# Kernel optimization log

Measured on AMD Instinct MI355X. Metric: run time of the kernel, lower is better.

Reference implementation:

```python
import jax, jax.numpy as jnp
import numpy as np

EPS = 1e-8

def setup_inputs() -> dict:
    key = jax.random.key(0)
    k1, k2 = jax.random.split(key)
    B, D, H, W, K = 32, 256, 64, 64, 64
    X = jax.random.normal(k1, (B, D, H, W), dtype=jnp.float32)
    std1 = 1.0 / float(np.sqrt(K * D))
    codewords = jax.random.uniform(k2, (K, D), dtype=jnp.float32, minval=-std1, maxval=std1)
    return {"X": X, "codewords": codewords}

def reference(X, codewords):
    B, D = X.shape[0], X.shape[1]
    # (B, D, H, W) -> (B, N, D)
    Xf = X.reshape(B, D, -1).transpose(0, 2, 1)
    # pairwise cosine similarity: normalize then matmul -> (B, N, K)
    Xn = Xf / jnp.maximum(jnp.linalg.norm(Xf, axis=-1, keepdims=True), EPS)
    Cn = codewords / jnp.maximum(jnp.linalg.norm(codewords, axis=-1, keepdims=True), EPS)
    L = jnp.einsum('bnd,kd->bnk', Xn, Cn)
    A = jax.nn.softmax(L, axis=2)
    # aggregate: E[b,k,d] = sum_n A[b,n,k] * (Xf[b,n,d] - C[k,d])
    # expressed without materializing the (B,N,K,D) residual tensor:
    E = jnp.einsum('bnk,bnd->bkd', A, Xf) - A.sum(axis=1)[:, :, None] * codewords[None, :, :]
    return E
```

## Files before the change

kernel.cpp:

```cpp
#include <hip/hip_runtime.h>
#include <hip/hip_bf16.h>
#include <math.h>

#define BB 32
#define DD 256
#define NN 4096
#define KK 64
#define EPSV 1e-8f
#define XSTR 264

typedef __attribute__((ext_vector_type(8))) short short8;
typedef __attribute__((ext_vector_type(4))) float f32x4;

__device__ __forceinline__ unsigned int bf16pair(float a, float b) {
    __hip_bfloat162 h = __float22bfloat162_rn(make_float2(a, b));
    return *(unsigned int*)&h;
}
__device__ __forceinline__ unsigned short bf16one(float a) {
    unsigned int ua = __float_as_uint(a);
    ua += 0x7fffu + ((ua >> 16) & 1u);
    return (unsigned short)(ua >> 16);
}

__device__ __forceinline__ void stage_group(int dbase, int n4, const float4* rr,
                                            unsigned short* xnd_s, unsigned short* xdn_s,
                                            f32x4& ssn) {
    float4 r0 = rr[0], r1 = rr[1], r2 = rr[2], r3 = rr[3];
    ssn.x = fmaf(r0.x, r0.x, ssn.x); ssn.x = fmaf(r1.x, r1.x, ssn.x);
    ssn.x = fmaf(r2.x, r2.x, ssn.x); ssn.x = fmaf(r3.x, r3.x, ssn.x);
    ssn.y = fmaf(r0.y, r0.y, ssn.y); ssn.y = fmaf(r1.y, r1.y, ssn.y);
    ssn.y = fmaf(r2.y, r2.y, ssn.y); ssn.y = fmaf(r3.y, r3.y, ssn.y);
    ssn.z = fmaf(r0.z, r0.z, ssn.z); ssn.z = fmaf(r1.z, r1.z, ssn.z);
    ssn.z = fmaf(r2.z, r2.z, ssn.z); ssn.z = fmaf(r3.z, r3.z, ssn.z);
    ssn.w = fmaf(r0.w, r0.w, ssn.w); ssn.w = fmaf(r1.w, r1.w, ssn.w);
    ssn.w = fmaf(r2.w, r2.w, ssn.w); ssn.w = fmaf(r3.w, r3.w, ssn.w);
#pragma unroll
    for (int j = 0; j < 4; j++) {
        int d = dbase + j;
        uint2 u;
        u.x = bf16pair(rr[j].x, rr[j].y);
        u.y = bf16pair(rr[j].z, rr[j].w);
        *(uint2*)(xdn_s + d * 64 + ((((n4 >> 3) ^ (d & 7)) << 3) | (n4 & 7))) = u;
    }
    {
        float col[4][4] = {{r0.x, r1.x, r2.x, r3.x},
                           {r0.y, r1.y, r2.y, r3.y},
                           {r0.z, r1.z, r2.z, r3.z},
                           {r0.w, r1.w, r2.w, r3.w}};
#pragma unroll
        for (int j = 0; j < 4; j++) {
            int n = n4 + j;
            uint2 u;
            u.x = bf16pair(col[j][0], col[j][1]);
            u.y = bf16pair(col[j][2], col[j][3]);
            int blk = (dbase >> 3) ^ ((n >> 2) & 3);
            *(uint2*)(xnd_s + n * XSTR + (blk << 3) + (dbase & 7)) = u;
        }
    }
}

__global__ __launch_bounds__(256, 2) void k_fused(const float* __restrict__ X,
                                                  const float* __restrict__ C,
                                                  float* __restrict__ P,
                                                  float* __restrict__ Sp) {
    __shared__ unsigned short xnd_s[64 * XSTR];
    __shared__ unsigned short xdn_s[DD * 64];
    __shared__ unsigned short at_s[KK * 72];
    __shared__ float rn4[4 * 64];
    __shared__ float red_s[4 * 64];

    int t = threadIdx.x;
    int b = blockIdx.x >> 4, chunk = blockIdx.x & 15;
    int w = t >> 6, lane = t & 63, c = lane & 15, g = lane >> 4;
    int q = t >> 4;
    int n4 = c * 4;

    const float* Xb = X + (size_t)b * DD * NN + chunk * 256;

    float4 pre[8];
#pragma unroll
    for (int i = 0; i < 2; i++) {
        const float* xb = Xb + (size_t)(q * 4 + 64 * i) * NN + n4;
#pragma unroll
        for (int j = 0; j < 4; j++) pre[i * 4 + j] = *(const float4*)(xb + (size_t)j * NN);
    }

    short8 cnf[8];
    {
        int k = 16 * w + c;
        const float* cp = C + k * DD;
        float4 v0[8], v1[8];
        float ss = 0.f;
#pragma unroll
        for (int ks = 0; ks < 8; ks++) {
            v0[ks] = *(const float4*)(cp + 32 * ks + 8 * g);
            v1[ks] = *(const float4*)(cp + 32 * ks + 8 * g + 4);
            ss = fmaf(v0[ks].x, v0[ks].x, ss); ss = fmaf(v0[ks].y, v0[ks].y, ss);
            ss = fmaf(v0[ks].z, v0[ks].z, ss); ss = fmaf(v0[ks].w, v0[ks].w, ss);
            ss = fmaf(v1[ks].x, v1[ks].x, ss); ss = fmaf(v1[ks].y, v1[ks].y, ss);
            ss = fmaf(v1[ks].z, v1[ks].z, ss); ss = fmaf(v1[ks].w, v1[ks].w, ss);
        }
        ss += __shfl_xor(ss, 16);
        ss += __shfl_xor(ss, 32);
        float r = 1.f / fmaxf(sqrtf(ss), EPSV);
#pragma unroll
        for (int ks = 0; ks < 8; ks++) {
            uint4 u;
            u.x = bf16pair(v0[ks].x * r, v0[ks].y * r);
            u.y = bf16pair(v0[ks].z * r, v0[ks].w * r);
            u.z = bf16pair(v1[ks].x * r, v1[ks].y * r);
            u.w = bf16pair(v1[ks].z * r, v1[ks].w * r);
            cnf[ks] = *(short8*)&u;
        }
    }

    f32x4 eacc[4][4];
#pragma unroll
    for (int dt = 0; dt < 4; dt++)
#pragma unroll
        for (int kt = 0; kt < 4; kt++) eacc[dt][kt] = (f32x4){0.f, 0.f, 0.f, 0.f};
    float s_acc[4] = {0.f, 0.f, 0.f, 0.f};

    for (int p = 0; p < 4; p++) {
        float4 cur[8];
#pragma unroll
        for (int i = 0; i < 2; i++) {
            const float* xb = Xb + (size_t)(q * 4 + 64 * (2 + i)) * NN + p * 64 + n4;
#pragma unroll
            for (int j = 0; j < 4; j++) cur[i * 4 + j] = *(const float4*)(xb + (size_t)j * NN);
        }
        __syncthreads();

        f32x4 ssn = (f32x4){0.f, 0.f, 0.f, 0.f};
#pragma unroll
        for (int i = 0; i < 2; i++)
            stage_group(q * 4 + 64 * i, n4, &pre[i * 4], xnd_s, xdn_s, ssn);
#pragma unroll
        for (int i = 0; i < 2; i++)
            stage_group(q * 4 + 64 * (2 + i), n4, &cur[i * 4], xnd_s, xdn_s, ssn);

        if (p < 3) {
#pragma unroll
            for (int i = 0; i < 2; i++) {
                const float* xb = Xb + (size_t)(q * 4 + 64 * i) * NN + (p + 1) * 64 + n4;
#pragma unroll
                for (int j = 0; j < 4; j++) pre[i * 4 + j] = *(const float4*)(xb + (size_t)j * NN);
            }
        }

        ssn.x += __shfl_xor(ssn.x, 16); ssn.x += __shfl_xor(ssn.x, 32);
        ssn.y += __shfl_xor(ssn.y, 16); ssn.y += __shfl_xor(ssn.y, 32);
        ssn.z += __shfl_xor(ssn.z, 16); ssn.z += __shfl_xor(ssn.z, 32);
        ssn.w += __shfl_xor(ssn.w, 16); ssn.w += __shfl_xor(ssn.w, 32);
        if (g == 0) *(f32x4*)(rn4 + w * 64 + n4) = ssn;

        __syncthreads();

        f32x4 lacc[4];
#pragma unroll
        for (int nt = 0; nt < 4; nt++) lacc[nt] = (f32x4){0.f, 0.f, 0.f, 0.f};
#pragma unroll
        for (int ks = 0; ks < 8; ks++) {
            short8 af = cnf[ks];
#pragma unroll
            for (int nt = 0; nt < 4; nt++) {
                int n = nt * 16 + c;
                short8 bf = *(const short8*)(xnd_s + n * XSTR +
                                             (((4 * ks + g) ^ ((n >> 2) & 3)) << 3));
                lacc[nt] = __builtin_amdgcn_mfma_f32_16x16x32_bf16(af, bf, lacc[nt], 0, 0, 0);
            }
        }

        float lv[4][4];
#pragma unroll
        for (int nt = 0; nt < 4; nt++) {
            int n = nt * 16 + c;
            float ssq = rn4[n] + rn4[64 + n] + rn4[128 + n] + rn4[192 + n];
            float rn = 1.f / fmaxf(sqrtf(ssq), EPSV);
            float s = 0.f;
#pragma unroll
            for (int r = 0; r < 4; r++) {
                lv[nt][r] = __expf(lacc[nt][r] * rn);
                s += lv[nt][r];
            }
            s += __shfl_xor(s, 16);
            s += __shfl_xor(s, 32);
            if (g == 0) red_s[w * 64 + n] = s;
        }
        __syncthreads();

#pragma unroll
        for (int nt = 0; nt < 4; nt++) {
            int n = nt * 16 + c;
            float denom = red_s[n] + red_s[64 + n] + red_s[128 + n] + red_s[192 + n];
            float inv = 1.f / denom;
#pragma unroll
            for (int r = 0; r < 4; r++) {
                float a = lv[nt][r] * inv;
                s_acc[r] += a;
                int k = 16 * w + 4 * g + r;
                at_s[k * 72 + ((((n >> 3) ^ (k & 7)) << 3) | (n & 7))] = bf16one(a);
            }
        }
        __syncthreads();

#pragma unroll
        for (int ks2 = 0; ks2 < 2; ks2++) {
            short8 bk[4];
#pragma unroll
            for (int kt = 0; kt < 4; kt++) {
                int k = kt * 16 + c;
                bk[kt] = *(const short8*)(at_s + k * 72 + (((4 * ks2 + g) ^ (k & 7)) << 3));
            }
#pragma unroll
            for (int dt = 0; dt < 4; dt++) {
                int d = w * 64 + dt * 16 + c;
                short8 af = *(const short8*)(xdn_s + d * 64 + (((4 * ks2 + g) ^ (d & 7)) << 3));
#pragma unroll
                for (int kt = 0; kt < 4; kt++)
                    eacc[dt][kt] =
                        __builtin_amdgcn_mfma_f32_16x16x32_bf16(af, bk[kt], eacc[dt][kt], 0, 0, 0);
            }
        }
    }

    float* Pb = P + (size_t)blockIdx.x * (DD * KK);
#pragma unroll
    for (int dt = 0; dt < 4; dt++)
#pragma unroll
        for (int kt = 0; kt < 4; kt++) {
            int k = kt * 16 + c;
            int d0 = w * 64 + dt * 16 + 4 * g;
            *(f32x4*)(Pb + (size_t)k * DD + d0) = eacc[dt][kt];
        }
#pragma unroll
    for (int r = 0; r < 4; r++) {
        float v = s_acc[r];
        v += __shfl_xor(v, 1);
        v += __shfl_xor(v, 2);
        v += __shfl_xor(v, 4);
        v += __shfl_xor(v, 8);
        if (c == 0) Sp[blockIdx.x * 64 + 16 * w + 4 * g + r] = v;
    }
}

__global__ __launch_bounds__(256) void k_fin(const float* __restrict__ P,
                                             const float* __restrict__ Sp,
                                             const float* __restrict__ C,
                                             float* __restrict__ out) {
    int idx = blockIdx.x * 256 + threadIdx.x;
    int b = idx >> 12;
    int r = idx & 4095;
    int k = r >> 6;
    int d0 = (r & 63) * 4;
    const float* Pp = P + (size_t)b * 16 * (DD * KK) + k * DD + d0;
    const float* Sb = Sp + b * 16 * 64 + k;
    f32x4 e0 = (f32x4){0.f, 0.f, 0.f, 0.f};
    f32x4 e1 = (f32x4){0.f, 0.f, 0.f, 0.f};
    float s0 = 0.f, s1 = 0.f;
#pragma unroll
    for (int cc = 0; cc < 16; cc += 2) {
        f32x4 p0 = *(const f32x4*)(Pp + (size_t)cc * (DD * KK));
        f32x4 p1 = *(const f32x4*)(Pp + (size_t)(cc + 1) * (DD * KK));
        e0 += p0;
        e1 += p1;
        s0 += Sb[cc * 64];
        s1 += Sb[(cc + 1) * 64];
    }
    f32x4 cv = *(const f32x4*)(C + k * DD + d0);
    f32x4 e = e0 + e1;
    float s = s0 + s1;
    f32x4 o;
    o.x = e.x - s * cv.x;
    o.y = e.y - s * cv.y;
    o.z = e.z - s * cv.z;
    o.w = e.w - s * cv.w;
    *(f32x4*)(out + (size_t)(b * 64 + k) * DD + d0) = o;
}

extern "C" void kernel_launch(void* const* d_in, const int* in_sizes, int n_in,
                              void* d_out, int out_size, void* d_ws, size_t ws_size,
                              hipStream_t stream) {
    const float* X = (const float*)d_in[0];
    const float* C = (const float*)d_in[1];
    float* out = (float*)d_out;
    unsigned char* ws = (unsigned char*)d_ws;

    float* Sp = (float*)ws;
    float* P = (float*)(ws + 131072);

    k_fused<<<512, 256, 0, stream>>>(X, C, P, Sp);
    k_fin<<<512, 256, 0, stream>>>(P, Sp, C, out);
}
```

Measured before the change: 211.3 us.

## Drop transposed LDS copy of X and feed aggregation MFMA from global loads

Removes the d-major bf16 shared-memory copy of the X tile (xdn_s) and its staging stores. The A-operand of the aggregation MFMA is instead built from fp32 X values reloaded from global memory (expected to hit L2) and converted to bf16 in registers. Dropping that buffer also allows the barrier at the top of each chunk loop to be removed. The trade is less LDS traffic and footprint against a second global read of X per tile and about 64 extra registers of live float4 data.

```diff
diff --git a/kernel.cpp b/kernel.cpp
--- a/kernel.cpp
+++ b/kernel.cpp
@@ -23,8 +23,7 @@
 }
 
 __device__ __forceinline__ void stage_group(int dbase, int n4, const float4* rr,
-                                            unsigned short* xnd_s, unsigned short* xdn_s,
-                                            f32x4& ssn) {
+                                            unsigned short* xnd_s, f32x4& ssn) {
     float4 r0 = rr[0], r1 = rr[1], r2 = rr[2], r3 = rr[3];
     ssn.x = fmaf(r0.x, r0.x, ssn.x); ssn.x = fmaf(r1.x, r1.x, ssn.x);
     ssn.x = fmaf(r2.x, r2.x, ssn.x); ssn.x = fmaf(r3.x, r3.x, ssn.x);
@@ -34,14 +33,6 @@
     ssn.z = fmaf(r2.z, r2.z, ssn.z); ssn.z = fmaf(r3.z, r3.z, ssn.z);
     ssn.w = fmaf(r0.w, r0.w, ssn.w); ssn.w = fmaf(r1.w, r1.w, ssn.w);
     ssn.w = fmaf(r2.w, r2.w, ssn.w); ssn.w = fmaf(r3.w, r3.w, ssn.w);
-#pragma unroll
-    for (int j = 0; j < 4; j++) {
-        int d = dbase + j;
-        uint2 u;
-        u.x = bf16pair(rr[j].x, rr[j].y);
-        u.y = bf16pair(rr[j].z, rr[j].w);
-        *(uint2*)(xdn_s + d * 64 + ((((n4 >> 3) ^ (d & 7)) << 3) | (n4 & 7))) = u;
-    }
     {
         float col[4][4] = {{r0.x, r1.x, r2.x, r3.x},
                            {r0.y, r1.y, r2.y, r3.y},
@@ -64,7 +55,6 @@
                                                   float* __restrict__ P,
                                                   float* __restrict__ Sp) {
     __shared__ unsigned short xnd_s[64 * XSTR];
-    __shared__ unsigned short xdn_s[DD * 64];
     __shared__ unsigned short at_s[KK * 72];
     __shared__ float rn4[4 * 64];
     __shared__ float red_s[4 * 64];
@@ -129,15 +119,14 @@
 #pragma unroll
             for (int j = 0; j < 4; j++) cur[i * 4 + j] = *(const float4*)(xb + (size_t)j * NN);
         }
-        __syncthreads();
 
         f32x4 ssn = (f32x4){0.f, 0.f, 0.f, 0.f};
 #pragma unroll
         for (int i = 0; i < 2; i++)
-            stage_group(q * 4 + 64 * i, n4, &pre[i * 4], xnd_s, xdn_s, ssn);
+            stage_group(q * 4 + 64 * i, n4, &pre[i * 4], xnd_s, ssn);
 #pragma unroll
         for (int i = 0; i < 2; i++)
-            stage_group(q * 4 + 64 * (2 + i), n4, &cur[i * 4], xnd_s, xdn_s, ssn);
+            stage_group(q * 4 + 64 * (2 + i), n4, &cur[i * 4], xnd_s, ssn);
 
         if (p < 3) {
 #pragma unroll
@@ -156,6 +145,14 @@
 
         __syncthreads();
 
+        float4 ax0[8];
+#pragma unroll
+        for (int dt = 0; dt < 4; dt++) {
+            const float* xa = Xb + (size_t)(w * 64 + dt * 16 + c) * NN + p * 64 + 8 * g;
+            ax0[dt * 2 + 0] = *(const float4*)(xa);
+            ax0[dt * 2 + 1] = *(const float4*)(xa + 4);
+        }
+
         f32x4 lacc[4];
 #pragma unroll
         for (int nt = 0; nt < 4; nt++) lacc[nt] = (f32x4){0.f, 0.f, 0.f, 0.f};
@@ -171,6 +168,14 @@
             }
         }
 
+        float4 ax1[8];
+#pragma unroll
+        for (int dt = 0; dt < 4; dt++) {
+            const float* xa = Xb + (size_t)(w * 64 + dt * 16 + c) * NN + p * 64 + 32 + 8 * g;
+            ax1[dt * 2 + 0] = *(const float4*)(xa);
+            ax1[dt * 2 + 1] = *(const float4*)(xa + 4);
+        }
+
         float lv[4][4];
 #pragma unroll
         for (int nt = 0; nt < 4; nt++) {
@@ -206,6 +211,7 @@
 
 #pragma unroll
         for (int ks2 = 0; ks2 < 2; ks2++) {
+            const float4* ax = (ks2 == 0) ? ax0 : ax1;
             short8 bk[4];
 #pragma unroll
             for (int kt = 0; kt < 4; kt++) {
@@ -214,8 +220,14 @@
             }
 #pragma unroll
             for (int dt = 0; dt < 4; dt++) {
-                int d = w * 64 + dt * 16 + c;
-                short8 af = *(const short8*)(xdn_s + d * 64 + (((4 * ks2 + g) ^ (d & 7)) << 3));
+                float4 f0 = ax[dt * 2 + 0];
+                float4 f1 = ax[dt * 2 + 1];
+                uint4 u;
+                u.x = bf16pair(f0.x, f0.y);
+                u.y = bf16pair(f0.z, f0.w);
+                u.z = bf16pair(f1.x, f1.y);
+                u.w = bf16pair(f1.z, f1.w);
+                short8 af = *(short8*)&u;
 #pragma unroll
                 for (int kt = 0; kt < 4; kt++)
                     eacc[dt][kt] =
```

New measurement: 225.8 us. +6.9%, slower.
